# Kernel optimization log

Hardware: AMD Instinct MI355X
Metric: run time of the kernel (lower is better)

The kernel has to match this reference:

```python
import jax, jax.numpy as jnp
import numpy as np

EPS = 1e-5

def _ln(x, g, b):
    mu = jnp.mean(x, axis=-1, keepdims=True)
    var = jnp.var(x, axis=-1, keepdims=True)
    return (x - mu) * jax.lax.rsqrt(var + EPS) * g + b

def setup_inputs() -> dict:
    key = jax.random.key(0)
    ks = jax.random.split(key, 8)
    B, S, D, DK, DV = 8, 2048, 1024, 128, 128
    sD = 1.0 / np.sqrt(D)
    sDV = 1.0 / np.sqrt(DV)
    sH = 1.0 / np.sqrt(4 * D)
    return {
        "x": jax.random.normal(ks[0], (B, S, D), jnp.float32),
        "ln1_g": jnp.ones((D,), jnp.float32),
        "ln1_b": jnp.zeros((D,), jnp.float32),
        "Wq": jax.random.normal(ks[1], (D, DK), jnp.float32) * sD,
        "bq": jnp.zeros((DK,), jnp.float32),
        "Wk": jax.random.normal(ks[2], (D, DK), jnp.float32) * sD,
        "bk": jnp.zeros((DK,), jnp.float32),
        "Wv": jax.random.normal(ks[3], (D, DV), jnp.float32) * sD,
        "bv": jnp.zeros((DV,), jnp.float32),
        "Wo": jax.random.normal(ks[4], (DV, D), jnp.float32) * sDV,
        "bo": jnp.zeros((D,), jnp.float32),
        "ln2_g": jnp.ones((D,), jnp.float32),
        "ln2_b": jnp.zeros((D,), jnp.float32),
        "W1": jax.random.normal(ks[5], (D, 4 * D), jnp.float32) * sD,
        "b1": jnp.zeros((4 * D,), jnp.float32),
        "W2": jax.random.normal(ks[6], (4 * D, D), jnp.float32) * sH,
        "b2": jnp.zeros((D,), jnp.float32),
    }

def reference(x, ln1_g, ln1_b, Wq, bq, Wk, bk, Wv, bv, Wo, bo, ln2_g, ln2_b, W1, b1, W2, b2):
    # Block.forward (scaling_test=None): pre-LN, naive full attention, residual MLP
    xn = _ln(x, ln1_g, ln1_b)                       # [B,S,D]
    q = xn @ Wq + bq                                # [B,S,DK]
    k = xn @ Wk + bk                                # [B,S,DK]
    v = xn @ Wv + bv                                # [B,S,DV]
    scale = 1.0 / np.sqrt(q.shape[-1])
    S = jnp.einsum("bqd,bkd->bqk", q, k) * scale    # [B,S,S] materialized scores
    A = jax.nn.softmax(S, axis=-1)
    H = jnp.einsum("bqk,bkv->bqv", A, v)            # [B,S,DV]
    y = xn + (H @ Wo + bo)                          # note: residual uses ln1(x), as in source
    h = _ln(y, ln2_g, ln2_b)
    mlp = jax.nn.gelu(h @ W1 + b1, approximate=False) @ W2 + b2
    return y + mlp
```

## Files before the change

### kernel.cpp

```cpp
#include <hip/hip_runtime.h>
#include <math.h>

#define M_TOT   16384
#define D_MODEL 1024
#define D_HEAD  128
#define SEQ     2048
#define NBATCH  8
#define D_FF    4096

typedef _Float16 f16x8 __attribute__((ext_vector_type(8)));
typedef _Float16 f16x4 __attribute__((ext_vector_type(4)));
typedef float    f32x4 __attribute__((ext_vector_type(4)));

#define ATT_SCALE 0.08838834764831845f

__device__ __forceinline__ void gload_lds16(const _Float16* g, _Float16* l) {
  __builtin_amdgcn_global_load_lds(
      (const __attribute__((address_space(1))) unsigned int*)g,
      (__attribute__((address_space(3))) unsigned int*)l, 16, 0, 0);
}
__device__ __forceinline__ unsigned short f16bits(float v) {
  union { _Float16 f; unsigned short u; } cv; cv.f = (_Float16)v; return cv.u;
}
__device__ __forceinline__ float gelu_f(float x) {
  const float t = 0.7978845608028654f * x * (1.0f + 0.044715f * x * x);
  const float e = __expf(2.0f * t);
  const float th = 1.0f - 2.0f / (e + 1.0f);
  return 0.5f * x * (1.0f + th);
}
__device__ __forceinline__ void bar_sync() {
  __asm__ volatile("" ::: "memory");
  __builtin_amdgcn_s_barrier();
  __asm__ volatile("" ::: "memory");
}
__device__ __forceinline__ int swzb(int row, int quad) {
  const int e = (((row & 1) << 2) | quad) ^ ((row >> 1) & 7);
  return ((row >> 1) << 7) | (e << 4);
}

__global__ __launch_bounds__(256) void convt_kernel(const float* __restrict__ in,
                                                    _Float16* __restrict__ out,
                                                    int K, int N) {
  __shared__ float t[32][33];
  const int n0 = blockIdx.x * 32, k0 = blockIdx.y * 32;
  const int tx = threadIdx.x & 31, ty = threadIdx.x >> 5;
#pragma unroll
  for (int r = 0; r < 4; r++)
    t[ty + 8 * r][tx] = in[(size_t)(k0 + ty + 8 * r) * N + n0 + tx];
  __syncthreads();
#pragma unroll
  for (int r = 0; r < 4; r++)
    out[(size_t)(n0 + ty + 8 * r) * K + k0 + tx] = (_Float16)t[tx][ty + 8 * r];
}

template <bool WF32>
__global__ __launch_bounds__(256) void ln_kernel(const float* __restrict__ in,
                                                 const float* __restrict__ gamma,
                                                 const float* __restrict__ beta,
                                                 float* __restrict__ of,
                                                 _Float16* __restrict__ oh) {
  __shared__ float shs[4], shq[4];
  const int row = blockIdx.x;
  const int t = threadIdx.x;
  float4 v = ((const float4*)(in + (size_t)row * D_MODEL))[t];
  float s = v.x + v.y + v.z + v.w;
  float q = v.x * v.x + v.y * v.y + v.z * v.z + v.w * v.w;
#pragma unroll
  for (int o = 32; o > 0; o >>= 1) {
    s += __shfl_down(s, o, 64);
    q += __shfl_down(q, o, 64);
  }
  const int lane = t & 63, w = t >> 6;
  if (lane == 0) { shs[w] = s; shq[w] = q; }
  __syncthreads();
  if (t == 0) {
    shs[0] = shs[0] + shs[1] + shs[2] + shs[3];
    shq[0] = shq[0] + shq[1] + shq[2] + shq[3];
  }
  __syncthreads();
  const float mu = shs[0] * (1.0f / D_MODEL);
  const float var = shq[0] * (1.0f / D_MODEL) - mu * mu;
  const float rs = rsqrtf(var + 1e-5f);
  float4 gv = ((const float4*)gamma)[t];
  float4 bv = ((const float4*)beta)[t];
  float4 o;
  o.x = (v.x - mu) * rs * gv.x + bv.x;
  o.y = (v.y - mu) * rs * gv.y + bv.y;
  o.z = (v.z - mu) * rs * gv.z + bv.z;
  o.w = (v.w - mu) * rs * gv.w + bv.w;
  if (WF32) ((float4*)(of + (size_t)row * D_MODEL))[t] = o;
  f16x4 h4 = {(_Float16)o.x, (_Float16)o.y, (_Float16)o.z, (_Float16)o.w};
  ((f16x4*)(oh + (size_t)row * D_MODEL))[t] = h4;
}


#define STAGE_A(JT)                                                       \
  {                                                                       \
    _Float16* ps_ = SM + (((JT) & 3) * 16384) + ldsA;                     \
    const size_t kp_ = (size_t)(JT) * 32;                                 \
    gload_lds16(Ag0 + kp_, ps_);                                          \
    gload_lds16(Ag0 + 16 * (size_t)K + kp_, ps_ + 512);                   \
  }
#define STAGE_B(JT)                                                       \
  {                                                                       \
    _Float16* ps_ = SM + (((JT) & 3) * 16384) + ldsB;                     \
    const size_t kp_ = (size_t)(JT) * 32;                                 \
    gload_lds16(Bg0 + kp_, ps_);                                          \
    gload_lds16(Bg0 + 16 * (size_t)K + kp_, ps_ + 512);                   \
  }

#define KTILE(JT, WSTR, PF)                                                    \
  {                                                                            \
    _Float16* sb_ = SM + (((JT) & 3) * 16384);                                 \
    const char* Ab_ = (const char*)sb_;                                        \
    const char* Bb_ = (const char*)(sb_ + 8192);                               \
    f16x8 af[8], bfr[4];                                                       \
    _Pragma("unroll") for (int m = 0; m < 8; ++m)                              \
        af[m] = *(const f16x8*)(Ab_ + swzb(wm * 128 + m * 16 + l15, quad));    \
    bfr[0] = *(const f16x8*)(Bb_ + swzb(wn * 64 + l15, quad));                 \
    bfr[1] = *(const f16x8*)(Bb_ + swzb(wn * 64 + 16 + l15, quad));            \
    if (PF) { STAGE_A((JT) + 3); }                                             \
    bar_sync();                                                                \
    asm volatile("s_waitcnt lgkmcnt(0)" ::: "memory");                         \
    __builtin_amdgcn_sched_barrier(0);                                         \
    __builtin_amdgcn_s_setprio(1);                                             \
    _Pragma("unroll") for (int m = 0; m < 8; ++m) {                            \
      acc[m][0] = __builtin_amdgcn_mfma_f32_16x16x32_f16(af[m], bfr[0], acc[m][0], 0, 0, 0); \
      acc[m][1] = __builtin_amdgcn_mfma_f32_16x16x32_f16(af[m], bfr[1], acc[m][1], 0, 0, 0); \
    }                                                                          \
    __builtin_amdgcn_s_setprio(0);                                             \
    bar_sync();                                                                \
    bfr[2] = *(const f16x8*)(Bb_ + swzb(wn * 64 + 32 + l15, quad));            \
    bfr[3] = *(const f16x8*)(Bb_ + swzb(wn * 64 + 48 + l15, quad));            \
    if (PF) { STAGE_B((JT) + 3); }                                             \
    asm volatile("s_waitcnt " WSTR ::: "memory");                              \
    bar_sync();                                                                \
    asm volatile("s_waitcnt lgkmcnt(0)" ::: "memory");                         \
    __builtin_amdgcn_sched_barrier(0);                                         \
    __builtin_amdgcn_s_setprio(1);                                             \
    _Pragma("unroll") for (int m = 0; m < 8; ++m) {                            \
      acc[m][2] = __builtin_amdgcn_mfma_f32_16x16x32_f16(af[m], bfr[2], acc[m][2], 0, 0, 0); \
      acc[m][3] = __builtin_amdgcn_mfma_f32_16x16x32_f16(af[m], bfr[3], acc[m][3], 0, 0, 0); \
    }                                                                          \
    __builtin_amdgcn_s_setprio(0);                                             \
    bar_sync();                                                                \
  }

template <int MODE>
__global__ __launch_bounds__(512, 2) void mfma_gemm256(
    const _Float16* __restrict__ A, const _Float16* __restrict__ BT,
    const float* __restrict__ bias, const float* __restrict__ res,
    void* __restrict__ Cout, int M, int N, int K) {
  __shared__ __attribute__((aligned(16))) _Float16 SM[4 * 16384];
  const int tid = threadIdx.x;
  const int lane = tid & 63, w = tid >> 6;
  const int l15 = lane & 15, quad = lane >> 4;
  const int wm = w >> 2, wn = w & 3;

  const int nwg = gridDim.x;
  const int bid = (blockIdx.x & 7) * (nwg >> 3) + (blockIdx.x >> 3);
  const int nbx = N >> 8;
  const int bx = bid % nbx, by = bid / nbx;
  const int row0 = by << 8, col0 = bx << 8;

  const int rp = lane >> 3;
  const int el = (lane & 7) ^ rp;
  const int lr = (rp << 1) | (el >> 2);
  const int lc = (el & 3) << 3;
  const _Float16* Ag0 = A + (size_t)(row0 + w * 32 + lr) * K + lc;
  const _Float16* Bg0 = BT + (size_t)(col0 + w * 32 + lr) * K + lc;
  const int ldsA = w * 1024;
  const int ldsB = 8192 + w * 1024;

  const f32x4 zero = {0.f, 0.f, 0.f, 0.f};
  f32x4 acc[8][4];
#pragma unroll
  for (int m = 0; m < 8; ++m)
#pragma unroll
    for (int n = 0; n < 4; ++n) acc[m][n] = zero;

  const int NKT = K >> 5;
  for (int t = 0; t < 3; ++t) { STAGE_A(t); STAGE_B(t); }
  asm volatile("s_waitcnt vmcnt(8)" ::: "memory");
  bar_sync();

  int j = 0;
#pragma unroll 1
  for (; j + 3 < NKT; ++j) { KTILE(j, "vmcnt(8)", 1); }
  KTILE(j, "vmcnt(4)", 0); ++j;
  KTILE(j, "vmcnt(0)", 0); ++j;
  KTILE(j, "vmcnt(0)", 0);

  const int colb = col0 + wn * 64 + l15;
  if (MODE == 0) {
    float* C = (float*)Cout;
    float bv[4];
#pragma unroll
    for (int n = 0; n < 4; ++n) bv[n] = bias[colb + n * 16];
#pragma unroll
    for (int m = 0; m < 8; ++m)
#pragma unroll
      for (int r = 0; r < 4; ++r) {
        const int row = row0 + wm * 128 + m * 16 + quad * 4 + r;
        const size_t base = (size_t)row * N + colb;
        const float* rp2 = res + base;
        float* cp = C + base;
#pragma unroll
        for (int n = 0; n < 4; ++n) cp[n * 16] = acc[m][n][r] + bv[n] + rp2[n * 16];
      }
  } else {
    _Float16* C = (_Float16*)Cout;
    float bv[4];
#pragma unroll
    for (int n = 0; n < 4; ++n) bv[n] = bias[colb + n * 16];
#pragma unroll
    for (int m = 0; m < 8; ++m)
#pragma unroll
      for (int r = 0; r < 4; ++r) {
        const int row = row0 + wm * 128 + m * 16 + quad * 4 + r;
        _Float16* cp = C + (size_t)row * N + colb;
#pragma unroll
        for (int n = 0; n < 4; ++n) cp[n * 16] = (_Float16)gelu_f(acc[m][n][r] + bv[n]);
      }
  }
  (void)M;
}

template <int MODE>
__global__ __launch_bounds__(256) void mfma_gemm(const _Float16* __restrict__ A,
                                                 const _Float16* __restrict__ BT,
                                                 const float* __restrict__ b0p,
                                                 const float* __restrict__ b1p,
                                                 const float* __restrict__ b2p,
                                                 const float* __restrict__ res,
                                                 void* __restrict__ Cout,
                                                 _Float16* __restrict__ vtout,
                                                 int M, int N, int K) {
  __shared__ _Float16 SMEM[2 * 128 * 32];
  _Float16* As = SMEM;
  _Float16* Bs = SMEM + 128 * 32;
  const int tid = threadIdx.x;
  const int lane = tid & 63, w = tid >> 6;
  const int wr = w >> 1, wc = w & 1;
  const int row0 = blockIdx.y << 7, col0 = blockIdx.x << 7;
  const int l15 = lane & 15, quad = lane >> 4;
  const f32x4 zero = {0.f, 0.f, 0.f, 0.f};
  f32x4 acc[4][4];
#pragma unroll
  for (int i = 0; i < 4; i++)
#pragma unroll
    for (int j = 0; j < 4; j++) acc[i][j] = zero;

  const int srow = lane >> 2;
  const int scol = (lane & 3) << 3;
  const _Float16* Ag = A + (size_t)(row0 + w * 32 + srow) * K + scol;
  const _Float16* Bg = BT + (size_t)(col0 + w * 32 + srow) * K + scol;

  for (int k0 = 0; k0 < K; k0 += 32) {
#pragma unroll
    for (int p = 0; p < 2; p++) {
      gload_lds16(Ag + (size_t)(p * 16) * K + k0, &As[(w * 32 + p * 16) * 32]);
      gload_lds16(Bg + (size_t)(p * 16) * K + k0, &Bs[(w * 32 + p * 16) * 32]);
    }
    __syncthreads();
    f16x8 af[4], bfr[4];
#pragma unroll
    for (int i = 0; i < 4; i++) {
      af[i]  = *(const f16x8*)&As[(wr * 64 + i * 16 + l15) * 32 + quad * 8];
      bfr[i] = *(const f16x8*)&Bs[(wc * 64 + i * 16 + l15) * 32 + quad * 8];
    }
#pragma unroll
    for (int i = 0; i < 4; i++)
#pragma unroll
      for (int j = 0; j < 4; j++)
        acc[i][j] = __builtin_amdgcn_mfma_f32_16x16x32_f16(af[i], bfr[j], acc[i][j], 0, 0, 0);
    __syncthreads();
  }

  if (MODE == 0) {
    float* C = (float*)Cout;
    float bv4[4];
#pragma unroll
    for (int j = 0; j < 4; j++) bv4[j] = b0p[col0 + wc * 64 + j * 16 + l15];
#pragma unroll
    for (int i = 0; i < 4; i++)
#pragma unroll
      for (int r = 0; r < 4; r++) {
        const int row = row0 + wr * 64 + i * 16 + quad * 4 + r;
        const size_t base = (size_t)row * N + col0 + wc * 64 + l15;
        const float* rp = res + base;
        float* cp = C + base;
#pragma unroll
        for (int j = 0; j < 4; j++)
          cp[j * 16] = acc[i][j][r] + bv4[j] + rp[j * 16];
      }
  } else if (MODE == 1) {
    _Float16* C = (_Float16*)Cout;
    float bv4[4];
#pragma unroll
    for (int j = 0; j < 4; j++) bv4[j] = b0p[col0 + wc * 64 + j * 16 + l15];
#pragma unroll
    for (int i = 0; i < 4; i++)
#pragma unroll
      for (int r = 0; r < 4; r++) {
        const int row = row0 + wr * 64 + i * 16 + quad * 4 + r;
        _Float16* cp = C + (size_t)row * N + col0 + wc * 64 + l15;
#pragma unroll
        for (int j = 0; j < 4; j++)
          cp[j * 16] = (_Float16)gelu_f(acc[i][j][r] + bv4[j]);
      }
  } else {
    _Float16* qkout = (_Float16*)Cout;
    const int bx = blockIdx.x;
    if (bx < 2) {
      const float* bp = (bx == 0) ? b0p : b1p;
      const float sc = (bx == 0) ? ATT_SCALE : 1.0f;
      const int cofs = bx * 128 + wc * 64 + l15;
      float bv4[4];
#pragma unroll
      for (int j = 0; j < 4; j++) bv4[j] = bp[wc * 64 + j * 16 + l15];
#pragma unroll
      for (int i = 0; i < 4; i++)
#pragma unroll
        for (int r = 0; r < 4; r++) {
          const int row = row0 + wr * 64 + i * 16 + quad * 4 + r;
          _Float16* cp = qkout + (size_t)row * 256 + cofs;
#pragma unroll
          for (int j = 0; j < 4; j++)
            cp[j * 16] = (_Float16)((acc[i][j][r] + bv4[j]) * sc);
        }
    } else {
      _Float16* Ts = SMEM;
      float bv4[4];
#pragma unroll
      for (int j = 0; j < 4; j++) bv4[j] = b2p[wc * 64 + j * 16 + l15];
      const int bb = row0 >> 11, s0 = row0 & 2047;
#pragma unroll
      for (int c = 0; c < 4; c++) {
        __syncthreads();
        if (wr == (c >> 1)) {
#pragma unroll
          for (int ii = 0; ii < 2; ii++) {
            const int i = (c & 1) * 2 + ii;
#pragma unroll
            for (int j = 0; j < 4; j++) {
              const int vd = wc * 64 + j * 16 + l15;
              const int slocal = ii * 16 + quad * 4;
              ushort4 h;
              h.x = f16bits(acc[i][j][0] + bv4[j]);
              h.y = f16bits(acc[i][j][1] + bv4[j]);
              h.z = f16bits(acc[i][j][2] + bv4[j]);
              h.w = f16bits(acc[i][j][3] + bv4[j]);
              *(ushort4*)&Ts[vd * 40 + slocal] = h;
            }
          }
        }
        __syncthreads();
#pragma unroll
        for (int p = 0; p < 2; p++) {
          const int idx = tid + p * 256;
          const int vd = idx >> 2, s8 = (idx & 3) * 8;
          uint4 d = *(const uint4*)&Ts[vd * 40 + s8];
          *(uint4*)&vtout[((size_t)bb * 128 + vd) * SEQ + s0 + c * 32 + s8] = d;
        }
      }
    }
  }
}

__global__ __launch_bounds__(256) void flash_attn_mfma(const _Float16* __restrict__ qk,
                                                       const _Float16* __restrict__ vt,
                                                       _Float16* __restrict__ H) {
  __shared__ _Float16 Ks[2][64][136];
  __shared__ _Float16 Vs[128][72];
  __shared__ _Float16 Ps[4][16][72];
  const int b = blockIdx.y, q0 = blockIdx.x * 64;
  const int tid = threadIdx.x;
  const int lane = tid & 63, w = tid >> 6;
  const int l15 = lane & 15, quad = lane >> 4;

  f16x8 qf[4];
  {
    const _Float16* qrow = qk + ((size_t)(b * SEQ + q0 + w * 16 + l15)) * 256 + quad * 8;
#pragma unroll
    for (int ks = 0; ks < 4; ks++) qf[ks] = *(const f16x8*)(qrow + ks * 32);
  }
  const f32x4 zero = {0.f, 0.f, 0.f, 0.f};
  f32x4 O[8];
#pragma unroll
  for (int i = 0; i < 8; i++) O[i] = zero;
  float m_r[4] = {-1e30f, -1e30f, -1e30f, -1e30f};
  float l_r[4] = {0.f, 0.f, 0.f, 0.f};

  const _Float16* kg0 = qk + (size_t)(b * SEQ) * 256 + 128 + (size_t)(tid >> 4) * 256 + (tid & 15) * 8;
  const _Float16* vg0 = vt + (size_t)b * 128 * SEQ + (size_t)((tid >> 3)) * SEQ + (tid & 7) * 8;
  uint4 kp[4], vp[4];

#define LOAD_TILE(kt)                                                            \
  {                                                                              \
    const _Float16* kg = kg0 + (size_t)(kt) * 64 * 256;                          \
    const _Float16* vg = vg0 + (size_t)(kt) * 64;                                \
    _Pragma("unroll") for (int p = 0; p < 4; p++) {                              \
      kp[p] = *(const uint4*)(kg + (size_t)p * 16 * 256);                        \
      vp[p] = *(const uint4*)(vg + (size_t)p * 32 * SEQ);                        \
    }                                                                            \
  }
#define STORE_K(buf)                                                             \
  _Pragma("unroll") for (int p = 0; p < 4; p++)                                  \
      *(uint4*)&Ks[buf][(tid >> 4) + 16 * p][(tid & 15) * 8] = kp[p];
#define STORE_V()                                                                \
  _Pragma("unroll") for (int p = 0; p < 4; p++)                                  \
      *(uint4*)&Vs[(tid >> 3) + 32 * p][(tid & 7) * 8] = vp[p];

  LOAD_TILE(0);
  STORE_K(0);
  STORE_V();
  __syncthreads();

  const int NT = SEQ / 64;
  for (int kt = 0; kt < NT; kt++) {
    const int cur = kt & 1;
    if (kt + 1 < NT) LOAD_TILE(kt + 1);

    f32x4 s4[4];
#pragma unroll
    for (int nt = 0; nt < 4; nt++) {
      s4[nt] = zero;
#pragma unroll
      for (int ks = 0; ks < 4; ks++) {
        f16x8 kf = *(const f16x8*)&Ks[cur][nt * 16 + l15][ks * 32 + quad * 8];
        s4[nt] = __builtin_amdgcn_mfma_f32_16x16x32_f16(qf[ks], kf, s4[nt], 0, 0, 0);
      }
    }
    float rmax[4], alpha[4], rsum[4];
#pragma unroll
    for (int r = 0; r < 4; r++)
      rmax[r] = fmaxf(fmaxf(s4[0][r], s4[1][r]), fmaxf(s4[2][r], s4[3][r]));
#pragma unroll
    for (int o = 1; o < 16; o <<= 1)
#pragma unroll
      for (int r = 0; r < 4; r++) rmax[r] = fmaxf(rmax[r], __shfl_xor(rmax[r], o, 64));
#pragma unroll
    for (int r = 0; r < 4; r++) {
      const float nm = fmaxf(m_r[r], rmax[r]);
      alpha[r] = __expf(m_r[r] - nm);
      m_r[r] = nm;
#pragma unroll
      for (int nt = 0; nt < 4; nt++) s4[nt][r] = __expf(s4[nt][r] - nm);
      rsum[r] = s4[0][r] + s4[1][r] + s4[2][r] + s4[3][r];
    }
#pragma unroll
    for (int o = 1; o < 16; o <<= 1)
#pragma unroll
      for (int r = 0; r < 4; r++) rsum[r] += __shfl_xor(rsum[r], o, 64);
#pragma unroll
    for (int r = 0; r < 4; r++) {
      l_r[r] = l_r[r] * alpha[r] + rsum[r];
#pragma unroll
      for (int i = 0; i < 8; i++) O[i][r] *= alpha[r];
    }
#pragma unroll
    for (int nt = 0; nt < 4; nt++)
#pragma unroll
      for (int r = 0; r < 4; r++)
        Ps[w][quad * 4 + r][nt * 16 + l15] = (_Float16)s4[nt][r];
    f16x8 pa[2];
#pragma unroll
    for (int ks = 0; ks < 2; ks++)
      pa[ks] = *(const f16x8*)&Ps[w][l15][ks * 32 + quad * 8];
#pragma unroll
    for (int ks = 0; ks < 2; ks++)
#pragma unroll
      for (int vt8 = 0; vt8 < 8; vt8++) {
        f16x8 vf = *(const f16x8*)&Vs[vt8 * 16 + l15][ks * 32 + quad * 8];
        O[vt8] = __builtin_amdgcn_mfma_f32_16x16x32_f16(pa[ks], vf, O[vt8], 0, 0, 0);
      }

    if (kt + 1 < NT) {
      STORE_K(cur ^ 1);
      __syncthreads();
      STORE_V();
      __syncthreads();
    }
  }
#pragma unroll
  for (int r = 0; r < 4; r++) {
    const float inv = 1.0f / l_r[r];
    _Float16* hp = H + (size_t)(b * SEQ + q0 + w * 16 + quad * 4 + r) * D_HEAD;
#pragma unroll
    for (int vt8 = 0; vt8 < 8; vt8++)
      hp[vt8 * 16 + l15] = (_Float16)(O[vt8][r] * inv);
  }
}

extern "C" void kernel_launch(void* const* d_in, const int* in_sizes, int n_in,
                              void* d_out, int out_size, void* d_ws, size_t ws_size,
                              hipStream_t stream) {
  const float* x     = (const float*)d_in[0];
  const float* ln1_g = (const float*)d_in[1];
  const float* ln1_b = (const float*)d_in[2];
  const float* Wq    = (const float*)d_in[3];
  const float* bq    = (const float*)d_in[4];
  const float* Wk    = (const float*)d_in[5];
  const float* bk    = (const float*)d_in[6];
  const float* Wv    = (const float*)d_in[7];
  const float* bv    = (const float*)d_in[8];
  const float* Wo    = (const float*)d_in[9];
  const float* bo    = (const float*)d_in[10];
  const float* ln2_g = (const float*)d_in[11];
  const float* ln2_b = (const float*)d_in[12];
  const float* W1    = (const float*)d_in[13];
  const float* b1    = (const float*)d_in[14];
  const float* W2    = (const float*)d_in[15];
  const float* b2    = (const float*)d_in[16];
  float* out = (float*)d_out;

  char* ws = (char*)d_ws;
  const size_t MB = 1024 * 1024;
  _Float16* W1T   = (_Float16*)(ws);
  _Float16* W2T   = (_Float16*)(ws + 8 * MB);
  _Float16* WqkvT = (_Float16*)(ws + 16 * MB);
  _Float16* WoT   = (_Float16*)(ws + 16 * MB + 768 * 1024);
  float*    xn_f32 = (float*)(ws + 20 * MB);
  _Float16* xn_f16 = (_Float16*)(ws + 84 * MB);
  _Float16* qkb  = (_Float16*)(ws + 116 * MB);
  _Float16* vtb  = (_Float16*)(ws + 124 * MB);
  _Float16* Hb   = (_Float16*)(ws + 128 * MB);
  _Float16* act  = (_Float16*)(ws + 20 * MB);
  _Float16* h16  = (_Float16*)(ws + 148 * MB);

  convt_kernel<<<dim3(D_FF / 32, D_MODEL / 32), 256, 0, stream>>>(W1, W1T, D_MODEL, D_FF);
  convt_kernel<<<dim3(D_MODEL / 32, D_FF / 32), 256, 0, stream>>>(W2, W2T, D_FF, D_MODEL);
  convt_kernel<<<dim3(D_HEAD / 32, D_MODEL / 32), 256, 0, stream>>>(Wq, WqkvT, D_MODEL, D_HEAD);
  convt_kernel<<<dim3(D_HEAD / 32, D_MODEL / 32), 256, 0, stream>>>(Wk, WqkvT + 128 * 1024, D_MODEL, D_HEAD);
  convt_kernel<<<dim3(D_HEAD / 32, D_MODEL / 32), 256, 0, stream>>>(Wv, WqkvT + 256 * 1024, D_MODEL, D_HEAD);
  convt_kernel<<<dim3(D_MODEL / 32, D_HEAD / 32), 256, 0, stream>>>(Wo, WoT, D_HEAD, D_MODEL);
  ln_kernel<true><<<dim3(M_TOT), 256, 0, stream>>>(x, ln1_g, ln1_b, xn_f32, xn_f16);
  mfma_gemm<2><<<dim3(3, M_TOT / 128), 256, 0, stream>>>(
      xn_f16, WqkvT, bq, bk, bv, nullptr, qkb, vtb, M_TOT, 384, D_MODEL);
  flash_attn_mfma<<<dim3(SEQ / 64, NBATCH), 256, 0, stream>>>(qkb, vtb, Hb);
  mfma_gemm256<0><<<dim3((D_MODEL / 256) * (M_TOT / 256)), 512, 0, stream>>>(
      Hb, WoT, bo, xn_f32, out, M_TOT, D_MODEL, D_HEAD);
  ln_kernel<false><<<dim3(M_TOT), 256, 0, stream>>>(out, ln2_g, ln2_b, nullptr, h16);
  mfma_gemm256<1><<<dim3((D_FF / 256) * (M_TOT / 256)), 512, 0, stream>>>(
      h16, W1T, b1, nullptr, act, M_TOT, D_FF, D_MODEL);
  mfma_gemm256<0><<<dim3((D_MODEL / 256) * (M_TOT / 256)), 512, 0, stream>>>(
      act, W2T, b2, out, out, M_TOT, D_MODEL, D_FF);

  (void)in_sizes; (void)n_in; (void)out_size; (void)ws_size;
}
```

Measured before the change: 663.8 us.

## Double-buffer register fragments to overlap LDS reads with MFMA in GEMM

Restructures the GEMM K-loop so the LDS fragments for tile j+1 are read into a second register set while the MFMAs for tile j run, with one barrier per K-tile instead of four. It also issues the A and B global-to-LDS prefetches together and uses inline-asm ds_read_b128 with immediate offsets and precomputed swizzled base addresses to cut address arithmetic. The cost is twice the fragment registers, which may push register pressure against the launch bound of two blocks per CU. The new loop also assumes the K-tile count parity fits the two-way unrolled main loop and epilogue.

```diff
diff --git a/kernel.cpp b/kernel.cpp
--- a/kernel.cpp
+++ b/kernel.cpp
@@ -36,6 +36,9 @@
 __device__ __forceinline__ int swzb(int row, int quad) {
   const int e = (((row & 1) << 2) | quad) ^ ((row >> 1) & 7);
   return ((row >> 1) << 7) | (e << 4);
+}
+__device__ __forceinline__ void ds_read128o(f16x8& d, unsigned addr, int imm) {
+  asm volatile("ds_read_b128 %0, %1 offset:%2" : "=v"(d) : "v"(addr), "i"(imm));
 }
 
 __global__ __launch_bounds__(256) void convt_kernel(const float* __restrict__ in,
@@ -94,6 +97,22 @@
 }
 
 
+struct Frag { f16x8 a[8]; f16x8 b[4]; };
+
+__device__ __forceinline__ void rd_frags(Frag& f, unsigned bA, unsigned bB) {
+#pragma unroll
+  for (int m = 0; m < 8; ++m) ds_read128o(f.a[m], bA, m * 1024);
+#pragma unroll
+  for (int n = 0; n < 4; ++n) ds_read128o(f.b[n], bB, n * 1024);
+}
+__device__ __forceinline__ void mfma32(f32x4 acc[8][4], const Frag& f) {
+#pragma unroll
+  for (int m = 0; m < 8; ++m)
+#pragma unroll
+    for (int n = 0; n < 4; ++n)
+      acc[m][n] = __builtin_amdgcn_mfma_f32_16x16x32_f16(f.a[m], f.b[n], acc[m][n], 0, 0, 0);
+}
+
 #define STAGE_A(JT)                                                       \
   {                                                                       \
     _Float16* ps_ = SM + (((JT) & 3) * 16384) + ldsA;                     \
@@ -109,41 +128,22 @@
     gload_lds16(Bg0 + 16 * (size_t)K + kp_, ps_ + 512);                   \
   }
 
-#define KTILE(JT, WSTR, PF)                                                    \
+#define KITER(CUR, NXT, JT, RD, PF, WVM)                                       \
   {                                                                            \
-    _Float16* sb_ = SM + (((JT) & 3) * 16384);                                 \
-    const char* Ab_ = (const char*)sb_;                                        \
-    const char* Bb_ = (const char*)(sb_ + 8192);                               \
-    f16x8 af[8], bfr[4];                                                       \
-    _Pragma("unroll") for (int m = 0; m < 8; ++m)                              \
-        af[m] = *(const f16x8*)(Ab_ + swzb(wm * 128 + m * 16 + l15, quad));    \
-    bfr[0] = *(const f16x8*)(Bb_ + swzb(wn * 64 + l15, quad));                 \
-    bfr[1] = *(const f16x8*)(Bb_ + swzb(wn * 64 + 16 + l15, quad));            \
-    if (PF) { STAGE_A((JT) + 3); }                                             \
-    bar_sync();                                                                \
     asm volatile("s_waitcnt lgkmcnt(0)" ::: "memory");                         \
     __builtin_amdgcn_sched_barrier(0);                                         \
-    __builtin_amdgcn_s_setprio(1);                                             \
-    _Pragma("unroll") for (int m = 0; m < 8; ++m) {                            \
-      acc[m][0] = __builtin_amdgcn_mfma_f32_16x16x32_f16(af[m], bfr[0], acc[m][0], 0, 0, 0); \
-      acc[m][1] = __builtin_amdgcn_mfma_f32_16x16x32_f16(af[m], bfr[1], acc[m][1], 0, 0, 0); \
+    bar_sync();                                                                \
+    if (RD) {                                                                  \
+      const unsigned sb_ = ((unsigned)(((JT) + 1) & 3)) << 15;                 \
+      rd_frags(NXT, fbaseA + sb_, fbaseB + sb_);                               \
     }                                                                          \
-    __builtin_amdgcn_s_setprio(0);                                             \
-    bar_sync();                                                                \
-    bfr[2] = *(const f16x8*)(Bb_ + swzb(wn * 64 + 32 + l15, quad));            \
-    bfr[3] = *(const f16x8*)(Bb_ + swzb(wn * 64 + 48 + l15, quad));            \
-    if (PF) { STAGE_B((JT) + 3); }                                             \
-    asm volatile("s_waitcnt " WSTR ::: "memory");                              \
-    bar_sync();                                                                \
-    asm volatile("s_waitcnt lgkmcnt(0)" ::: "memory");                         \
+    if (PF) { STAGE_A((JT) + 3); STAGE_B((JT) + 3); }                          \
     __builtin_amdgcn_sched_barrier(0);                                         \
     __builtin_amdgcn_s_setprio(1);                                             \
-    _Pragma("unroll") for (int m = 0; m < 8; ++m) {                            \
-      acc[m][2] = __builtin_amdgcn_mfma_f32_16x16x32_f16(af[m], bfr[2], acc[m][2], 0, 0, 0); \
-      acc[m][3] = __builtin_amdgcn_mfma_f32_16x16x32_f16(af[m], bfr[3], acc[m][3], 0, 0, 0); \
-    }                                                                          \
+    mfma32(acc, CUR);                                                          \
     __builtin_amdgcn_s_setprio(0);                                             \
-    bar_sync();                                                                \
+    if ((WVM) == 4) { asm volatile("s_waitcnt vmcnt(4)" ::: "memory"); bar_sync(); } \
+    if ((WVM) == 0) { asm volatile("s_waitcnt vmcnt(0)" ::: "memory"); bar_sync(); } \
   }
 
 template <int MODE>
@@ -172,6 +172,13 @@
   const int ldsA = w * 1024;
   const int ldsB = 8192 + w * 1024;
 
+  const unsigned lds0 =
+      (unsigned)(size_t)(__attribute__((address_space(3))) _Float16*)&SM[0];
+  const unsigned esw = (unsigned)((((l15 & 1) << 2) | quad) ^ ((l15 >> 1) & 7));
+  const unsigned rl128 = (unsigned)(l15 >> 1) << 7;
+  const unsigned fbaseA = lds0 + (unsigned)(wm * 8192) + rl128 + (esw << 4);
+  const unsigned fbaseB = lds0 + 16384u + (unsigned)(wn * 4096) + rl128 + (esw << 4);
+
   const f32x4 zero = {0.f, 0.f, 0.f, 0.f};
   f32x4 acc[8][4];
 #pragma unroll
@@ -180,16 +187,23 @@
     for (int n = 0; n < 4; ++n) acc[m][n] = zero;
 
   const int NKT = K >> 5;
+  Frag fA, fB;
+
   for (int t = 0; t < 3; ++t) { STAGE_A(t); STAGE_B(t); }
-  asm volatile("s_waitcnt vmcnt(8)" ::: "memory");
+  asm volatile("s_waitcnt vmcnt(4)" ::: "memory");
   bar_sync();
+  rd_frags(fA, fbaseA, fbaseB);
 
   int j = 0;
 #pragma unroll 1
-  for (; j + 3 < NKT; ++j) { KTILE(j, "vmcnt(8)", 1); }
-  KTILE(j, "vmcnt(4)", 0); ++j;
-  KTILE(j, "vmcnt(0)", 0); ++j;
-  KTILE(j, "vmcnt(0)", 0);
+  for (; j + 5 < NKT; j += 2) {
+    KITER(fA, fB, j,     1, 1, 4);
+    KITER(fB, fA, j + 1, 1, 1, 4);
+  }
+  KITER(fA, fB, NKT - 4, 1, 1, 4);
+  KITER(fB, fA, NKT - 3, 1, 0, 0);
+  KITER(fA, fB, NKT - 2, 1, 0, -1);
+  KITER(fB, fA, NKT - 1, 0, 0, -1);
 
   const int colb = col0 + wn * 64 + l15;
   if (MODE == 0) {
```

Measured after the change: 646.5 us. 2.6% less time.
